# Kernel tuning notes

Hardware: AMD Instinct MI355X
Metric: run time of the kernel (lower is better)

The kernel has to match this reference:

```python
import jax, jax.numpy as jnp
import numpy as np

N_NODES = 50000
N_EDGES = 600000
IN_DIM = 128
HID = 128
OUT_DIM = 2


def _init_linear(key, out_dim, in_dim):
    scale = 1.0 / np.sqrt(in_dim)
    return jax.random.uniform(key, (out_dim, in_dim), jnp.float32, -scale, scale)


def setup_inputs() -> dict:
    key = jax.random.key(0)
    ks = jax.random.split(key, 12)
    x = jax.random.normal(ks[0], (N_NODES, IN_DIM), jnp.float32)
    edge_index = jax.random.randint(ks[1], (2, N_EDGES), 0, N_NODES, jnp.int64)
    dims = [(HID, IN_DIM), (HID, HID), (OUT_DIM, HID)]
    inp = {"x": x, "edge_index": edge_index}
    for i, (o, d) in enumerate(dims):
        inp[f"Wl{i}"] = _init_linear(ks[2 + 3 * i], o, d)      # lin_l: applied to aggregated neighbors
        inp[f"Wr{i}"] = _init_linear(ks[3 + 3 * i], o, d)      # lin_r: applied to root (self) features
        inp[f"b{i}"] = jnp.zeros((o,), jnp.float32)            # bias of lin_l
    return inp


def _sage_conv(x, src, dst, Wl, Wr, b):
    # mean-aggregate source features onto target nodes, then linear transform
    msgs = x[src]                                              # [E, d] gather
    agg = jax.ops.segment_sum(msgs, dst, num_segments=N_NODES)
    cnt = jax.ops.segment_sum(jnp.ones((src.shape[0], 1), x.dtype), dst,
                              num_segments=N_NODES)
    agg = agg / jnp.maximum(cnt, 1.0)                          # mean over in-edges
    return agg @ Wl.T + b + x @ Wr.T


def reference(x, edge_index, Wl0, Wr0, b0, Wl1, Wr1, b1, Wl2, Wr2, b2):
    src, dst = edge_index[0], edge_index[1]
    # eval mode: dropout is identity
    h = jax.nn.relu(_sage_conv(x, src, dst, Wl0, Wr0, b0))
    h = jax.nn.relu(_sage_conv(h, src, dst, Wl1, Wr1, b1))
    return _sage_conv(h, src, dst, Wl2, Wr2, b2)
```

## Files before the change

### kernel.cpp

```cpp
#include <hip/hip_runtime.h>
#include <hip/hip_bf16.h>

#define N_NODES 50000
#define N_EDGES 600000
#define DIM 128
#define CAP 64

typedef short bf16x8 __attribute__((ext_vector_type(8)));
typedef float f32x4 __attribute__((ext_vector_type(4)));

__device__ __forceinline__ ushort f2b(float f) {
    __hip_bfloat16 h = __float2bfloat16(f);
    return *reinterpret_cast<ushort*>(&h);
}
__device__ __forceinline__ float b2f_lo(unsigned u) { return __uint_as_float(u << 16); }
__device__ __forceinline__ float b2f_hi(unsigned u) { return __uint_as_float(u & 0xffff0000u); }

static constexpr size_t alignup(size_t x) { return (x + 255) & ~size_t(255); }
static constexpr size_t OFF_FLAG = 0;
static constexpr size_t OFF_CNT  = 256;
static constexpr size_t OFF_COL  = alignup(OFF_CNT + sizeof(unsigned) * N_NODES);
static constexpr size_t OFF_XBF  = alignup(OFF_COL + sizeof(int) * (size_t)N_NODES * CAP);
static constexpr size_t OFF_AGG  = alignup(OFF_XBF + sizeof(ushort) * N_NODES * DIM);
static constexpr size_t OFF_H1   = alignup(OFF_AGG + sizeof(ushort) * N_NODES * DIM);
static constexpr size_t OFF_Z    = alignup(OFF_H1 + sizeof(ushort) * N_NODES * DIM);
static constexpr size_t OFF_RT   = alignup(OFF_Z + sizeof(float) * 2 * N_NODES);
static constexpr size_t OFF_WL0  = alignup(OFF_RT + sizeof(float) * 2 * N_NODES);
static constexpr size_t OFF_WR0  = alignup(OFF_WL0 + sizeof(ushort) * DIM * DIM);
static constexpr size_t OFF_WL1  = alignup(OFF_WR0 + sizeof(ushort) * DIM * DIM);
static constexpr size_t OFF_WR1  = alignup(OFF_WL1 + sizeof(ushort) * DIM * DIM);

__global__ __launch_bounds__(256) void prep_k(const int* __restrict__ ei,
                                              const float* __restrict__ x,
                                              const float* __restrict__ wa, const float* __restrict__ wb,
                                              const float* __restrict__ wc, const float* __restrict__ wd,
                                              unsigned* __restrict__ flag,
                                              unsigned* __restrict__ cnt,
                                              ushort* __restrict__ xbf,
                                              ushort* __restrict__ oa, ushort* __restrict__ ob,
                                              ushort* __restrict__ oc, ushort* __restrict__ od) {
    const int bid = blockIdx.x, t = threadIdx.x;
    if (bid < 6250) {
        const int i = bid * 256 + t;
        float4 v = reinterpret_cast<const float4*>(x)[i];
        ushort4 o;
        o.x = f2b(v.x); o.y = f2b(v.y); o.z = f2b(v.z); o.w = f2b(v.w);
        reinterpret_cast<ushort4*>(xbf)[i] = o;
        if (i < N_NODES) cnt[i] = 0u;
        if (bid == 0) {
            __shared__ unsigned any;
            if (t == 0) any = 0u;
            __syncthreads();
            unsigned hv = 0;
#pragma unroll
            for (int j = 0; j < 4; ++j) hv |= (unsigned)ei[2 * (t * 4 + j) + 1];
            if (hv) atomicOr(&any, 1u);
            __syncthreads();
            if (t == 0) *flag = any;
        }
    } else {
        const int wb_i = bid - 6250;
        const int w = wb_i >> 4;
        const float* src = (w == 0) ? wa : (w == 1) ? wb : (w == 2) ? wc : wd;
        ushort* dst      = (w == 0) ? oa : (w == 1) ? ob : (w == 2) ? oc : od;
        const int i = (wb_i & 15) * 256 + t;
        float4 v = reinterpret_cast<const float4*>(src)[i];
        ushort4 o;
        o.x = f2b(v.x); o.y = f2b(v.y); o.z = f2b(v.z); o.w = f2b(v.w);
        reinterpret_cast<ushort4*>(dst)[i] = o;
    }
}

__global__ void fillcsr_k(const int* __restrict__ ei, const unsigned* __restrict__ flag,
                          unsigned* __restrict__ cnt, int* __restrict__ col) {
    int e0 = (blockIdx.x * 256 + threadIdx.x) * 4;
    if (e0 >= N_EDGES) return;
    int s[4], d[4];
    if (*flag) {
        uint4 sv = *reinterpret_cast<const uint4*>(&ei[e0]);
        uint4 dv = *reinterpret_cast<const uint4*>(&ei[N_EDGES + e0]);
        s[0] = sv.x; s[1] = sv.y; s[2] = sv.z; s[3] = sv.w;
        d[0] = dv.x; d[1] = dv.y; d[2] = dv.z; d[3] = dv.w;
    } else {
        uint4 sa = *reinterpret_cast<const uint4*>(&ei[2 * e0]);
        uint4 sb = *reinterpret_cast<const uint4*>(&ei[2 * e0 + 4]);
        uint4 da = *reinterpret_cast<const uint4*>(&ei[2 * (N_EDGES + e0)]);
        uint4 db = *reinterpret_cast<const uint4*>(&ei[2 * (N_EDGES + e0) + 4]);
        s[0] = sa.x; s[1] = sa.z; s[2] = sb.x; s[3] = sb.z;
        d[0] = da.x; d[1] = da.z; d[2] = db.x; d[3] = db.z;
    }
#pragma unroll
    for (int i = 0; i < 4; ++i) {
        unsigned pos = atomicAdd(&cnt[d[i]], 1u);
        if (pos < CAP) col[(size_t)d[i] * CAP + pos] = s[i];
    }
}

__global__ __launch_bounds__(256) void agg_k(const ushort* __restrict__ h,
                                             const unsigned* __restrict__ cnt,
                                             const int* __restrict__ col,
                                             ushort* __restrict__ aggm) {
    const int wave = threadIdx.x >> 6;
    const int l    = threadIdx.x & 63;
    const int node = blockIdx.x * 4 + wave;
    unsigned deg = cnt[node];
    if (deg > CAP) deg = CAP;
    const int* cp = &col[(size_t)node * CAP];
    const int co = l * 2;
    float a0 = 0.f, a1 = 0.f;
    unsigned e = 0;
    for (; e + 4 <= deg; e += 4) {
        const int s0 = cp[e], s1 = cp[e + 1], s2 = cp[e + 2], s3 = cp[e + 3];
        const unsigned v0 = *reinterpret_cast<const unsigned*>(&h[(size_t)s0 * DIM + co]);
        const unsigned v1 = *reinterpret_cast<const unsigned*>(&h[(size_t)s1 * DIM + co]);
        const unsigned v2 = *reinterpret_cast<const unsigned*>(&h[(size_t)s2 * DIM + co]);
        const unsigned v3 = *reinterpret_cast<const unsigned*>(&h[(size_t)s3 * DIM + co]);
        a0 += b2f_lo(v0) + b2f_lo(v1) + b2f_lo(v2) + b2f_lo(v3);
        a1 += b2f_hi(v0) + b2f_hi(v1) + b2f_hi(v2) + b2f_hi(v3);
    }
    for (; e < deg; ++e) {
        const unsigned v = *reinterpret_cast<const unsigned*>(&h[(size_t)cp[e] * DIM + co]);
        a0 += b2f_lo(v); a1 += b2f_hi(v);
    }
    const float inv = 1.0f / fmaxf((float)deg, 1.0f);
    const unsigned o = (unsigned)f2b(a0 * inv) | ((unsigned)f2b(a1 * inv) << 16);
    *reinterpret_cast<unsigned*>(&aggm[(size_t)node * DIM + co]) = o;
}

__global__ __launch_bounds__(256) void xform_mfma_k(const ushort* __restrict__ A0,
                                                    const ushort* __restrict__ A1,
                                                    const ushort* __restrict__ Wl,
                                                    const ushort* __restrict__ Wr,
                                                    const float*  __restrict__ bias,
                                                    ushort* __restrict__ hout) {
    __shared__ ushort Ws[128 * 136];
    const int t    = threadIdx.x;
    const int wave = t >> 6;
    const int l    = t & 63;
    const int l16  = l & 15;
    const int lk   = (l >> 4) * 8;
    const int n0   = blockIdx.x * 128 + wave * 32 + l16;
    const int n1   = n0 + 16;
    const bool v0 = n0 < N_NODES, v1 = n1 < N_NODES;

    const int wrow = t >> 1;
    const int wc0  = (t & 1) * 64;

    f32x4 acc[2][8];
#pragma unroll
    for (int b = 0; b < 2; ++b)
#pragma unroll
        for (int i = 0; i < 8; ++i) acc[b][i] = (f32x4){0.f, 0.f, 0.f, 0.f};

    const bf16x8 zfrag = (bf16x8){0, 0, 0, 0, 0, 0, 0, 0};

#pragma unroll
    for (int p = 0; p < 2; ++p) {
        const ushort* Asrc = p ? A1 : A0;
        const ushort* Wsrc = p ? Wr : Wl;

        bf16x8 bf0[4], bf1[4];
#pragma unroll
        for (int ks = 0; ks < 4; ++ks) {
            bf0[ks] = v0 ? *reinterpret_cast<const bf16x8*>(&Asrc[(size_t)n0 * DIM + ks * 32 + lk]) : zfrag;
            bf1[ks] = v1 ? *reinterpret_cast<const bf16x8*>(&Asrc[(size_t)n1 * DIM + ks * 32 + lk]) : zfrag;
        }

        __syncthreads();
        {
            const uint4* src = reinterpret_cast<const uint4*>(&Wsrc[(size_t)wrow * DIM + wc0]);
            uint4* dst = reinterpret_cast<uint4*>(&Ws[wrow * 136 + wc0]);
#pragma unroll
            for (int i = 0; i < 8; ++i) dst[i] = src[i];
        }
        __syncthreads();

#pragma unroll
        for (int ks = 0; ks < 4; ++ks) {
            const int kb = ks * 32;
#pragma unroll
            for (int ot = 0; ot < 8; ++ot) {
                const bf16x8 afrag = *reinterpret_cast<const bf16x8*>(
                    &Ws[(ot * 16 + l16) * 136 + kb + lk]);
                acc[0][ot] = __builtin_amdgcn_mfma_f32_16x16x32_bf16(afrag, bf0[ks], acc[0][ot], 0, 0, 0);
                acc[1][ot] = __builtin_amdgcn_mfma_f32_16x16x32_bf16(afrag, bf1[ks], acc[1][ot], 0, 0, 0);
            }
        }
    }

    const int orow = (l >> 4) * 4;
#pragma unroll
    for (int b = 0; b < 2; ++b) {
        const int node = n0 + b * 16;
        if (node >= N_NODES) continue;
#pragma unroll
        for (int ot = 0; ot < 8; ++ot) {
            const float4 b4 = *reinterpret_cast<const float4*>(&bias[ot * 16 + orow]);
            float r0 = fmaxf(acc[b][ot][0] + b4.x, 0.f);
            float r1 = fmaxf(acc[b][ot][1] + b4.y, 0.f);
            float r2 = fmaxf(acc[b][ot][2] + b4.z, 0.f);
            float r3 = fmaxf(acc[b][ot][3] + b4.w, 0.f);
            ushort4 s;
            s.x = f2b(r0); s.y = f2b(r1); s.z = f2b(r2); s.w = f2b(r3);
            *reinterpret_cast<ushort4*>(&hout[(size_t)node * DIM + ot * 16 + orow]) = s;
        }
    }
}

__global__ __launch_bounds__(256) void xform_final_k(const ushort* __restrict__ A0,
                                                     const ushort* __restrict__ A1,
                                                     const ushort* __restrict__ Wl,
                                                     const ushort* __restrict__ Wr,
                                                     const float*  __restrict__ bias,
                                                     const float*  __restrict__ Wl2,
                                                     const float*  __restrict__ Wr2,
                                                     const float*  __restrict__ b2,
                                                     float* __restrict__ z,
                                                     float* __restrict__ rt) {
    __shared__ ushort Ws[128 * 136];
    __shared__ float wl2s[256], wr2s[256];
    const int t    = threadIdx.x;
    const int wave = t >> 6;
    const int l    = t & 63;
    const int l16  = l & 15;
    const int lk   = (l >> 4) * 8;
    const int n0   = blockIdx.x * 128 + wave * 32 + l16;
    const int n1   = n0 + 16;
    const bool v0 = n0 < N_NODES, v1 = n1 < N_NODES;

    const int wrow = t >> 1;
    const int wc0  = (t & 1) * 64;

    wl2s[t] = Wl2[t];
    wr2s[t] = Wr2[t];

    f32x4 acc[2][8];
#pragma unroll
    for (int b = 0; b < 2; ++b)
#pragma unroll
        for (int i = 0; i < 8; ++i) acc[b][i] = (f32x4){0.f, 0.f, 0.f, 0.f};

    const bf16x8 zfrag = (bf16x8){0, 0, 0, 0, 0, 0, 0, 0};

#pragma unroll
    for (int p = 0; p < 2; ++p) {
        const ushort* Asrc = p ? A1 : A0;
        const ushort* Wsrc = p ? Wr : Wl;

        bf16x8 bf0[4], bf1[4];
#pragma unroll
        for (int ks = 0; ks < 4; ++ks) {
            bf0[ks] = v0 ? *reinterpret_cast<const bf16x8*>(&Asrc[(size_t)n0 * DIM + ks * 32 + lk]) : zfrag;
            bf1[ks] = v1 ? *reinterpret_cast<const bf16x8*>(&Asrc[(size_t)n1 * DIM + ks * 32 + lk]) : zfrag;
        }

        __syncthreads();
        {
            const uint4* src = reinterpret_cast<const uint4*>(&Wsrc[(size_t)wrow * DIM + wc0]);
            uint4* dst = reinterpret_cast<uint4*>(&Ws[wrow * 136 + wc0]);
#pragma unroll
            for (int i = 0; i < 8; ++i) dst[i] = src[i];
        }
        __syncthreads();

#pragma unroll
        for (int ks = 0; ks < 4; ++ks) {
            const int kb = ks * 32;
#pragma unroll
            for (int ot = 0; ot < 8; ++ot) {
                const bf16x8 afrag = *reinterpret_cast<const bf16x8*>(
                    &Ws[(ot * 16 + l16) * 136 + kb + lk]);
                acc[0][ot] = __builtin_amdgcn_mfma_f32_16x16x32_bf16(afrag, bf0[ks], acc[0][ot], 0, 0, 0);
                acc[1][ot] = __builtin_amdgcn_mfma_f32_16x16x32_bf16(afrag, bf1[ks], acc[1][ot], 0, 0, 0);
            }
        }
    }

    const int orow = (l >> 4) * 4;
#pragma unroll
    for (int b = 0; b < 2; ++b) {
        float z0 = 0.f, z1 = 0.f, r0s = 0.f, r1s = 0.f;
#pragma unroll
        for (int ot = 0; ot < 8; ++ot) {
            const int o = ot * 16 + orow;
            const float4 b4 = *reinterpret_cast<const float4*>(&bias[o]);
            const float h0 = fmaxf(acc[b][ot][0] + b4.x, 0.f);
            const float h1v = fmaxf(acc[b][ot][1] + b4.y, 0.f);
            const float h2v = fmaxf(acc[b][ot][2] + b4.z, 0.f);
            const float h3 = fmaxf(acc[b][ot][3] + b4.w, 0.f);
            z0  += h0 * wl2s[o] + h1v * wl2s[o + 1] + h2v * wl2s[o + 2] + h3 * wl2s[o + 3];
            z1  += h0 * wl2s[128 + o] + h1v * wl2s[128 + o + 1] + h2v * wl2s[128 + o + 2] + h3 * wl2s[128 + o + 3];
            r0s += h0 * wr2s[o] + h1v * wr2s[o + 1] + h2v * wr2s[o + 2] + h3 * wr2s[o + 3];
            r1s += h0 * wr2s[128 + o] + h1v * wr2s[128 + o + 1] + h2v * wr2s[128 + o + 2] + h3 * wr2s[128 + o + 3];
        }
        z0  += __shfl_xor(z0, 16);  z0  += __shfl_xor(z0, 32);
        z1  += __shfl_xor(z1, 16);  z1  += __shfl_xor(z1, 32);
        r0s += __shfl_xor(r0s, 16); r0s += __shfl_xor(r0s, 32);
        r1s += __shfl_xor(r1s, 16); r1s += __shfl_xor(r1s, 32);
        const int node = n0 + b * 16;
        if ((l >> 4) == 0 && node < N_NODES) {
            float2 zv = {z0, z1};
            float2 rv = {r0s + b2[0], r1s + b2[1]};
            *reinterpret_cast<float2*>(&z[(size_t)node * 2])  = zv;
            *reinterpret_cast<float2*>(&rt[(size_t)node * 2]) = rv;
        }
    }
}

__global__ __launch_bounds__(256) void outgather_k(const float* __restrict__ z,
                                                   const float* __restrict__ rt,
                                                   const unsigned* __restrict__ cnt,
                                                   const int* __restrict__ col,
                                                   float* __restrict__ out) {
    const int g = threadIdx.x >> 3, lane = threadIdx.x & 7;
    const int node = blockIdx.x * 32 + g;
    if (node >= N_NODES) return;
    unsigned deg = cnt[node];
    if (deg > CAP) deg = CAP;
    const int* cp = &col[(size_t)node * CAP];
    float s0 = 0.f, s1 = 0.f;
    for (unsigned e = lane; e < deg; e += 8) {
        const int s = cp[e];
        const float2 v = *reinterpret_cast<const float2*>(&z[(size_t)s * 2]);
        s0 += v.x; s1 += v.y;
    }
#pragma unroll
    for (int m = 1; m < 8; m <<= 1) {
        s0 += __shfl_xor(s0, m);
        s1 += __shfl_xor(s1, m);
    }
    if (lane == 0) {
        const float inv = 1.0f / fmaxf((float)deg, 1.0f);
        const float2 rv = *reinterpret_cast<const float2*>(&rt[(size_t)node * 2]);
        float2 o = {s0 * inv + rv.x, s1 * inv + rv.y};
        *reinterpret_cast<float2*>(&out[(size_t)node * 2]) = o;
    }
}

extern "C" void kernel_launch(void* const* d_in, const int* in_sizes, int n_in,
                              void* d_out, int out_size, void* d_ws, size_t ws_size,
                              hipStream_t stream) {
    const float* x   = (const float*)d_in[0];
    const int*   ei  = (const int*)d_in[1];
    const float* Wl0 = (const float*)d_in[2];
    const float* Wr0 = (const float*)d_in[3];
    const float* b0  = (const float*)d_in[4];
    const float* Wl1 = (const float*)d_in[5];
    const float* Wr1 = (const float*)d_in[6];
    const float* b1  = (const float*)d_in[7];
    const float* Wl2 = (const float*)d_in[8];
    const float* Wr2 = (const float*)d_in[9];
    const float* b2  = (const float*)d_in[10];

    char* ws = (char*)d_ws;
    unsigned* flag = (unsigned*)(ws + OFF_FLAG);
    unsigned* cnt  = (unsigned*)(ws + OFF_CNT);
    int*      col  = (int*)(ws + OFF_COL);
    ushort*   xbf  = (ushort*)(ws + OFF_XBF);
    ushort*   aggm = (ushort*)(ws + OFF_AGG);
    ushort*   h1   = (ushort*)(ws + OFF_H1);
    float*    zbuf = (float*)(ws + OFF_Z);
    float*    rtb  = (float*)(ws + OFF_RT);
    ushort*   wl0b = (ushort*)(ws + OFF_WL0);
    ushort*   wr0b = (ushort*)(ws + OFF_WR0);
    ushort*   wl1b = (ushort*)(ws + OFF_WL1);
    ushort*   wr1b = (ushort*)(ws + OFF_WR1);
    float*    out  = (float*)d_out;

    prep_k<<<6250 + 64, 256, 0, stream>>>(ei, x, Wl0, Wr0, Wl1, Wr1,
                                          flag, cnt, xbf, wl0b, wr0b, wl1b, wr1b);
    fillcsr_k<<<(N_EDGES / 4 + 255) / 256, 256, 0, stream>>>(ei, flag, cnt, col);

    agg_k<<<N_NODES / 4, 256, 0, stream>>>(xbf, cnt, col, aggm);
    xform_mfma_k<<<(N_NODES + 127) / 128, 256, 0, stream>>>(aggm, xbf, wl0b, wr0b, b0, h1);
    agg_k<<<N_NODES / 4, 256, 0, stream>>>(h1, cnt, col, aggm);
    xform_final_k<<<(N_NODES + 127) / 128, 256, 0, stream>>>(aggm, h1, wl1b, wr1b, b1,
                                                             Wl2, Wr2, b2, zbuf, rtb);
    outgather_k<<<(N_NODES + 31) / 32, 256, 0, stream>>>(zbuf, rtb, cnt, col, out);
}
```

Baseline: 143.1 us.

## Sort CSR neighbor lists and widen aggregation to 16-lane groups with 16-byte loads

Adds a per-node bitonic sort of the neighbor lists after CSR build, so the accumulation order no longer depends on atomic insertion order and source rows are visited in address order. The aggregation kernel now uses 16 lanes per node with uint4 (8 bf16) loads instead of 64 lanes with 4-byte loads, so each wave processes four nodes and issues fewer, wider gather requests. The cost is one extra kernel launch and a pass over the column array, plus more registers per thread.

Result: slower. 146.8 us (+2.6%).

```diff
diff --git a/kernel.cpp b/kernel.cpp
--- a/kernel.cpp
+++ b/kernel.cpp
@@ -96,35 +96,73 @@
     }
 }
 
+__global__ __launch_bounds__(256) void sortcsr_k(const unsigned* __restrict__ cnt,
+                                                 int* __restrict__ col) {
+    const int wave = threadIdx.x >> 6;
+    const int l    = threadIdx.x & 63;
+    const int node = blockIdx.x * 4 + wave;
+    if (node >= N_NODES) return;
+    unsigned deg = cnt[node];
+    if (deg > CAP) deg = CAP;
+    if (deg <= 1) return;
+    int key = (l < (int)deg) ? col[(size_t)node * CAP + l] : 0x7fffffff;
+#pragma unroll
+    for (int k = 2; k <= 64; k <<= 1) {
+#pragma unroll
+        for (int j = k >> 1; j > 0; j >>= 1) {
+            const int partner = __shfl_xor(key, j);
+            const bool keepMin = (((l & k) == 0) == ((l & j) == 0));
+            key = keepMin ? min(key, partner) : max(key, partner);
+        }
+    }
+    if (l < (int)deg) col[(size_t)node * CAP + l] = key;
+}
+
 __global__ __launch_bounds__(256) void agg_k(const ushort* __restrict__ h,
                                              const unsigned* __restrict__ cnt,
                                              const int* __restrict__ col,
                                              ushort* __restrict__ aggm) {
-    const int wave = threadIdx.x >> 6;
-    const int l    = threadIdx.x & 63;
-    const int node = blockIdx.x * 4 + wave;
+    const int g = threadIdx.x >> 4, lane = threadIdx.x & 15;
+    const int node = blockIdx.x * 16 + g;
+    if (node >= N_NODES) return;
     unsigned deg = cnt[node];
     if (deg > CAP) deg = CAP;
     const int* cp = &col[(size_t)node * CAP];
-    const int co = l * 2;
-    float a0 = 0.f, a1 = 0.f;
+    float acc[8];
+#pragma unroll
+    for (int i = 0; i < 8; ++i) acc[i] = 0.f;
+    const int co = lane * 8;
     unsigned e = 0;
     for (; e + 4 <= deg; e += 4) {
         const int s0 = cp[e], s1 = cp[e + 1], s2 = cp[e + 2], s3 = cp[e + 3];
-        const unsigned v0 = *reinterpret_cast<const unsigned*>(&h[(size_t)s0 * DIM + co]);
-        const unsigned v1 = *reinterpret_cast<const unsigned*>(&h[(size_t)s1 * DIM + co]);
-        const unsigned v2 = *reinterpret_cast<const unsigned*>(&h[(size_t)s2 * DIM + co]);
-        const unsigned v3 = *reinterpret_cast<const unsigned*>(&h[(size_t)s3 * DIM + co]);
-        a0 += b2f_lo(v0) + b2f_lo(v1) + b2f_lo(v2) + b2f_lo(v3);
-        a1 += b2f_hi(v0) + b2f_hi(v1) + b2f_hi(v2) + b2f_hi(v3);
+        const uint4 v0 = *reinterpret_cast<const uint4*>(&h[(size_t)s0 * DIM + co]);
+        const uint4 v1 = *reinterpret_cast<const uint4*>(&h[(size_t)s1 * DIM + co]);
+        const uint4 v2 = *reinterpret_cast<const uint4*>(&h[(size_t)s2 * DIM + co]);
+        const uint4 v3 = *reinterpret_cast<const uint4*>(&h[(size_t)s3 * DIM + co]);
+        acc[0] += b2f_lo(v0.x) + b2f_lo(v1.x) + b2f_lo(v2.x) + b2f_lo(v3.x);
+        acc[1] += b2f_hi(v0.x) + b2f_hi(v1.x) + b2f_hi(v2.x) + b2f_hi(v3.x);
+        acc[2] += b2f_lo(v0.y) + b2f_lo(v1.y) + b2f_lo(v2.y) + b2f_lo(v3.y);
+        acc[3] += b2f_hi(v0.y) + b2f_hi(v1.y) + b2f_hi(v2.y) + b2f_hi(v3.y);
+        acc[4] += b2f_lo(v0.z) + b2f_lo(v1.z) + b2f_lo(v2.z) + b2f_lo(v3.z);
+        acc[5] += b2f_hi(v0.z) + b2f_hi(v1.z) + b2f_hi(v2.z) + b2f_hi(v3.z);
+        acc[6] += b2f_lo(v0.w) + b2f_lo(v1.w) + b2f_lo(v2.w) + b2f_lo(v3.w);
+        acc[7] += b2f_hi(v0.w) + b2f_hi(v1.w) + b2f_hi(v2.w) + b2f_hi(v3.w);
     }
     for (; e < deg; ++e) {
-        const unsigned v = *reinterpret_cast<const unsigned*>(&h[(size_t)cp[e] * DIM + co]);
-        a0 += b2f_lo(v); a1 += b2f_hi(v);
+        const int s = cp[e];
+        const uint4 v = *reinterpret_cast<const uint4*>(&h[(size_t)s * DIM + co]);
+        acc[0] += b2f_lo(v.x); acc[1] += b2f_hi(v.x);
+        acc[2] += b2f_lo(v.y); acc[3] += b2f_hi(v.y);
+        acc[4] += b2f_lo(v.z); acc[5] += b2f_hi(v.z);
+        acc[6] += b2f_lo(v.w); acc[7] += b2f_hi(v.w);
     }
     const float inv = 1.0f / fmaxf((float)deg, 1.0f);
-    const unsigned o = (unsigned)f2b(a0 * inv) | ((unsigned)f2b(a1 * inv) << 16);
-    *reinterpret_cast<unsigned*>(&aggm[(size_t)node * DIM + co]) = o;
+    uint4 o;
+    o.x = (unsigned)f2b(acc[0] * inv) | ((unsigned)f2b(acc[1] * inv) << 16);
+    o.y = (unsigned)f2b(acc[2] * inv) | ((unsigned)f2b(acc[3] * inv) << 16);
+    o.z = (unsigned)f2b(acc[4] * inv) | ((unsigned)f2b(acc[5] * inv) << 16);
+    o.w = (unsigned)f2b(acc[6] * inv) | ((unsigned)f2b(acc[7] * inv) << 16);
+    *reinterpret_cast<uint4*>(&aggm[(size_t)node * DIM + co]) = o;
 }
 
 __global__ __launch_bounds__(256) void xform_mfma_k(const ushort* __restrict__ A0,
@@ -370,10 +408,11 @@
     prep_k<<<6250 + 64, 256, 0, stream>>>(ei, x, Wl0, Wr0, Wl1, Wr1,
                                           flag, cnt, xbf, wl0b, wr0b, wl1b, wr1b);
     fillcsr_k<<<(N_EDGES / 4 + 255) / 256, 256, 0, stream>>>(ei, flag, cnt, col);
-
-    agg_k<<<N_NODES / 4, 256, 0, stream>>>(xbf, cnt, col, aggm);
+    sortcsr_k<<<(N_NODES + 3) / 4, 256, 0, stream>>>(cnt, col);
+
+    agg_k<<<(N_NODES + 15) / 16, 256, 0, stream>>>(xbf, cnt, col, aggm);
     xform_mfma_k<<<(N_NODES + 127) / 128, 256, 0, stream>>>(aggm, xbf, wl0b, wr0b, b0, h1);
-    agg_k<<<N_NODES / 4, 256, 0, stream>>>(h1, cnt, col, aggm);
+    agg_k<<<(N_NODES + 15) / 16, 256, 0, stream>>>(h1, cnt, col, aggm);
     xform_final_k<<<(N_NODES + 127) / 128, 256, 0, stream>>>(aggm, h1, wl1b, wr1b, b1,
                                                              Wl2, Wr2, b2, zbuf, rtb);
     outgather_k<<<(N_NODES + 31) / 32, 256, 0, stream>>>(zbuf, rtb, cnt, col, out);
```

## Use 16-lane groups with 128-bit gathers and fixed-point integer accumulation in aggregation

Applied to the files above, without the earlier changes.

The neighbor aggregation kernel now gives each node 16 lanes that each load 8 bf16 values with one 128-bit load, instead of a 64-lane wave loading 2 values per lane. This raises bytes per memory request and fits more nodes per block. Sums are built as fixed-point integers, scaled by 2^16 in aggregation and 2^28 in the output gather, so the result no longer depends on summation order. The conversions add ALU work, and the output gather now uses 64-bit integers and double-precision math, which adds cost and can overflow or lose precision on large values.

Measured after the change: 135.4 us. 5.4% less time.

```diff
diff --git a/kernel.cpp b/kernel.cpp
--- a/kernel.cpp
+++ b/kernel.cpp
@@ -15,6 +15,9 @@
 }
 __device__ __forceinline__ float b2f_lo(unsigned u) { return __uint_as_float(u << 16); }
 __device__ __forceinline__ float b2f_hi(unsigned u) { return __uint_as_float(u & 0xffff0000u); }
+
+#define AGG_SCALE 65536.0f
+#define OUT_SCALE 268435456.0
 
 static constexpr size_t alignup(size_t x) { return (x + 255) & ~size_t(255); }
 static constexpr size_t OFF_FLAG = 0;
@@ -100,31 +103,59 @@
                                              const unsigned* __restrict__ cnt,
                                              const int* __restrict__ col,
                                              ushort* __restrict__ aggm) {
-    const int wave = threadIdx.x >> 6;
-    const int l    = threadIdx.x & 63;
-    const int node = blockIdx.x * 4 + wave;
+    const int g = threadIdx.x >> 4, lane = threadIdx.x & 15;
+    const int node = blockIdx.x * 16 + g;
+    if (node >= N_NODES) return;
     unsigned deg = cnt[node];
     if (deg > CAP) deg = CAP;
     const int* cp = &col[(size_t)node * CAP];
-    const int co = l * 2;
-    float a0 = 0.f, a1 = 0.f;
+    int acc[8];
+#pragma unroll
+    for (int i = 0; i < 8; ++i) acc[i] = 0;
+    const int co = lane * 8;
     unsigned e = 0;
     for (; e + 4 <= deg; e += 4) {
         const int s0 = cp[e], s1 = cp[e + 1], s2 = cp[e + 2], s3 = cp[e + 3];
-        const unsigned v0 = *reinterpret_cast<const unsigned*>(&h[(size_t)s0 * DIM + co]);
-        const unsigned v1 = *reinterpret_cast<const unsigned*>(&h[(size_t)s1 * DIM + co]);
-        const unsigned v2 = *reinterpret_cast<const unsigned*>(&h[(size_t)s2 * DIM + co]);
-        const unsigned v3 = *reinterpret_cast<const unsigned*>(&h[(size_t)s3 * DIM + co]);
-        a0 += b2f_lo(v0) + b2f_lo(v1) + b2f_lo(v2) + b2f_lo(v3);
-        a1 += b2f_hi(v0) + b2f_hi(v1) + b2f_hi(v2) + b2f_hi(v3);
+        const uint4 v0 = *reinterpret_cast<const uint4*>(&h[(size_t)s0 * DIM + co]);
+        const uint4 v1 = *reinterpret_cast<const uint4*>(&h[(size_t)s1 * DIM + co]);
+        const uint4 v2 = *reinterpret_cast<const uint4*>(&h[(size_t)s2 * DIM + co]);
+        const uint4 v3 = *reinterpret_cast<const uint4*>(&h[(size_t)s3 * DIM + co]);
+        acc[0] += __float2int_rn(b2f_lo(v0.x) * AGG_SCALE) + __float2int_rn(b2f_lo(v1.x) * AGG_SCALE)
+                + __float2int_rn(b2f_lo(v2.x) * AGG_SCALE) + __float2int_rn(b2f_lo(v3.x) * AGG_SCALE);
+        acc[1] += __float2int_rn(b2f_hi(v0.x) * AGG_SCALE) + __float2int_rn(b2f_hi(v1.x) * AGG_SCALE)
+                + __float2int_rn(b2f_hi(v2.x) * AGG_SCALE) + __float2int_rn(b2f_hi(v3.x) * AGG_SCALE);
+        acc[2] += __float2int_rn(b2f_lo(v0.y) * AGG_SCALE) + __float2int_rn(b2f_lo(v1.y) * AGG_SCALE)
+                + __float2int_rn(b2f_lo(v2.y) * AGG_SCALE) + __float2int_rn(b2f_lo(v3.y) * AGG_SCALE);
+        acc[3] += __float2int_rn(b2f_hi(v0.y) * AGG_SCALE) + __float2int_rn(b2f_hi(v1.y) * AGG_SCALE)
+                + __float2int_rn(b2f_hi(v2.y) * AGG_SCALE) + __float2int_rn(b2f_hi(v3.y) * AGG_SCALE);
+        acc[4] += __float2int_rn(b2f_lo(v0.z) * AGG_SCALE) + __float2int_rn(b2f_lo(v1.z) * AGG_SCALE)
+                + __float2int_rn(b2f_lo(v2.z) * AGG_SCALE) + __float2int_rn(b2f_lo(v3.z) * AGG_SCALE);
+        acc[5] += __float2int_rn(b2f_hi(v0.z) * AGG_SCALE) + __float2int_rn(b2f_hi(v1.z) * AGG_SCALE)
+                + __float2int_rn(b2f_hi(v2.z) * AGG_SCALE) + __float2int_rn(b2f_hi(v3.z) * AGG_SCALE);
+        acc[6] += __float2int_rn(b2f_lo(v0.w) * AGG_SCALE) + __float2int_rn(b2f_lo(v1.w) * AGG_SCALE)
+                + __float2int_rn(b2f_lo(v2.w) * AGG_SCALE) + __float2int_rn(b2f_lo(v3.w) * AGG_SCALE);
+        acc[7] += __float2int_rn(b2f_hi(v0.w) * AGG_SCALE) + __float2int_rn(b2f_hi(v1.w) * AGG_SCALE)
+                + __float2int_rn(b2f_hi(v2.w) * AGG_SCALE) + __float2int_rn(b2f_hi(v3.w) * AGG_SCALE);
     }
     for (; e < deg; ++e) {
-        const unsigned v = *reinterpret_cast<const unsigned*>(&h[(size_t)cp[e] * DIM + co]);
-        a0 += b2f_lo(v); a1 += b2f_hi(v);
-    }
-    const float inv = 1.0f / fmaxf((float)deg, 1.0f);
-    const unsigned o = (unsigned)f2b(a0 * inv) | ((unsigned)f2b(a1 * inv) << 16);
-    *reinterpret_cast<unsigned*>(&aggm[(size_t)node * DIM + co]) = o;
+        const int s = cp[e];
+        const uint4 v = *reinterpret_cast<const uint4*>(&h[(size_t)s * DIM + co]);
+        acc[0] += __float2int_rn(b2f_lo(v.x) * AGG_SCALE);
+        acc[1] += __float2int_rn(b2f_hi(v.x) * AGG_SCALE);
+        acc[2] += __float2int_rn(b2f_lo(v.y) * AGG_SCALE);
+        acc[3] += __float2int_rn(b2f_hi(v.y) * AGG_SCALE);
+        acc[4] += __float2int_rn(b2f_lo(v.z) * AGG_SCALE);
+        acc[5] += __float2int_rn(b2f_hi(v.z) * AGG_SCALE);
+        acc[6] += __float2int_rn(b2f_lo(v.w) * AGG_SCALE);
+        acc[7] += __float2int_rn(b2f_hi(v.w) * AGG_SCALE);
+    }
+    const float s = 1.0f / (AGG_SCALE * fmaxf((float)deg, 1.0f));
+    uint4 o;
+    o.x = (unsigned)f2b((float)acc[0] * s) | ((unsigned)f2b((float)acc[1] * s) << 16);
+    o.y = (unsigned)f2b((float)acc[2] * s) | ((unsigned)f2b((float)acc[3] * s) << 16);
+    o.z = (unsigned)f2b((float)acc[4] * s) | ((unsigned)f2b((float)acc[5] * s) << 16);
+    o.w = (unsigned)f2b((float)acc[6] * s) | ((unsigned)f2b((float)acc[7] * s) << 16);
+    *reinterpret_cast<uint4*>(&aggm[(size_t)node * DIM + co]) = o;
 }
 
 __global__ __launch_bounds__(256) void xform_mfma_k(const ushort* __restrict__ A0,
@@ -318,11 +349,12 @@
     unsigned deg = cnt[node];
     if (deg > CAP) deg = CAP;
     const int* cp = &col[(size_t)node * CAP];
-    float s0 = 0.f, s1 = 0.f;
+    long long s0 = 0, s1 = 0;
     for (unsigned e = lane; e < deg; e += 8) {
         const int s = cp[e];
         const float2 v = *reinterpret_cast<const float2*>(&z[(size_t)s * 2]);
-        s0 += v.x; s1 += v.y;
+        s0 += __float2ll_rn(v.x * (float)OUT_SCALE);
+        s1 += __float2ll_rn(v.y * (float)OUT_SCALE);
     }
 #pragma unroll
     for (int m = 1; m < 8; m <<= 1) {
@@ -330,9 +362,9 @@
         s1 += __shfl_xor(s1, m);
     }
     if (lane == 0) {
-        const float inv = 1.0f / fmaxf((float)deg, 1.0f);
+        const double inv = 1.0 / (OUT_SCALE * (double)(deg > 0 ? deg : 1u));
         const float2 rv = *reinterpret_cast<const float2*>(&rt[(size_t)node * 2]);
-        float2 o = {s0 * inv + rv.x, s1 * inv + rv.y};
+        float2 o = {(float)((double)s0 * inv) + rv.x, (float)((double)s1 * inv) + rv.y};
         *reinterpret_cast<float2*>(&out[(size_t)node * 2]) = o;
     }
 }
@@ -371,9 +403,9 @@
                                           flag, cnt, xbf, wl0b, wr0b, wl1b, wr1b);
     fillcsr_k<<<(N_EDGES / 4 + 255) / 256, 256, 0, stream>>>(ei, flag, cnt, col);
 
-    agg_k<<<N_NODES / 4, 256, 0, stream>>>(xbf, cnt, col, aggm);
+    agg_k<<<(N_NODES + 15) / 16, 256, 0, stream>>>(xbf, cnt, col, aggm);
     xform_mfma_k<<<(N_NODES + 127) / 128, 256, 0, stream>>>(aggm, xbf, wl0b, wr0b, b0, h1);
-    agg_k<<<N_NODES / 4, 256, 0, stream>>>(h1, cnt, col, aggm);
+    agg_k<<<(N_NODES + 15) / 16, 256, 0, stream>>>(h1, cnt, col, aggm);
     xform_final_k<<<(N_NODES + 127) / 128, 256, 0, stream>>>(aggm, h1, wl1b, wr1b, b1,
                                                              Wl2, Wr2, b2, zbuf, rtb);
     outgather_k<<<(N_NODES + 31) / 32, 256, 0, stream>>>(zbuf, rtb, cnt, col, out);
```
